# Kernel optimization log

Hardware: AMD Instinct MI355X
Metric: run time of the kernel (lower is better)

Reference implementation:

```python
import jax, jax.numpy as jnp
import numpy as np

N_NODES = 100_000
N_EDGES = 1_600_000
NEG_SLOPE = 0.2

# layer configs: (in_channels, heads, out_channels, has_proj)
LAYERS = [(193, 8, 16, True), (128, 8, 16, False), (128, 8, 16, False), (128, 8, 8, True)]


def _gat_params(key, fin, H, C):
    ks = jax.random.split(key, 6)
    s = 1.0 / np.sqrt(fin)
    Wl = jax.random.normal(ks[0], (fin, H * C), dtype=jnp.float32) * s
    bl = jax.random.normal(ks[1], (H * C,), dtype=jnp.float32) * 0.01
    Wr = jax.random.normal(ks[2], (fin, H * C), dtype=jnp.float32) * s
    br = jax.random.normal(ks[3], (H * C,), dtype=jnp.float32) * 0.01
    att = jax.random.normal(ks[4], (H, C), dtype=jnp.float32) * (1.0 / np.sqrt(C))
    bias = jax.random.normal(ks[5], (H * C,), dtype=jnp.float32) * 0.01
    return Wl, bl, Wr, br, att, bias


def setup_inputs() -> dict:
    key = jax.random.key(0)
    ks = jax.random.split(key, 16)
    inp = {}
    inp['x'] = jax.random.normal(ks[0], (N_NODES, 193), dtype=jnp.float32)
    inp['edge_index'] = jax.random.randint(ks[1], (2, N_EDGES), 0, N_NODES, dtype=jnp.int64)
    for li, (fin, H, C, _) in enumerate(LAYERS, start=1):
        Wl, bl, Wr, br, att, bias = _gat_params(ks[1 + li], fin, H, C)
        inp[f'Wl{li}'] = Wl; inp[f'bl{li}'] = bl
        inp[f'Wr{li}'] = Wr; inp[f'br{li}'] = br
        inp[f'att{li}'] = att; inp[f'bias{li}'] = bias
    # residual projections where in_channels != heads*out_channels
    inp['proj1_W'] = jax.random.normal(ks[8], (193, 128), dtype=jnp.float32) * (1.0 / np.sqrt(193))
    inp['proj1_b'] = jax.random.normal(ks[9], (128,), dtype=jnp.float32) * 0.01
    inp['proj4_W'] = jax.random.normal(ks[10], (128, 64), dtype=jnp.float32) * (1.0 / np.sqrt(128))
    inp['proj4_b'] = jax.random.normal(ks[11], (64,), dtype=jnp.float32) * 0.01
    inp['lin1_W'] = jax.random.normal(ks[12], (64, 32), dtype=jnp.float32) * (1.0 / np.sqrt(64))
    inp['lin1_b'] = jax.random.normal(ks[13], (32,), dtype=jnp.float32) * 0.01
    return inp


def _gatv2(x, src, dst, Wl, bl, Wr, br, att, bias):
    # x: [N, Fin]; att: [H, C]
    N = x.shape[0]
    H, C = att.shape
    xl = (x @ Wl + bl).reshape(N, H, C)  # source transform
    xr = (x @ Wr + br).reshape(N, H, C)  # destination transform
    m = xl[src] + xr[dst]                # [E, H, C] edge gather
    e = jnp.einsum('ehc,hc->eh', jax.nn.leaky_relu(m, NEG_SLOPE), att)  # [E, H]
    emax = jax.ops.segment_max(e, dst, num_segments=N)  # per-dst softmax max
    p = jnp.exp(e - emax[dst])
    denom = jax.ops.segment_sum(p, dst, num_segments=N)
    alpha = p / (denom[dst] + 1e-16)     # [E, H]
    out = jax.ops.segment_sum(alpha[:, :, None] * xl[src], dst, num_segments=N)  # [N, H, C]
    return out.reshape(N, H * C) + bias


def _forward(x, edge_index, params):
    src, dst = edge_index[0], edge_index[1]
    h = x
    for li in range(4):
        Wl, bl, Wr, br, att, bias, projW, projb = params[li]
        g = _gatv2(h, src, dst, Wl, bl, Wr, br, att, bias)
        res = h @ projW + projb if projW is not None else h
        h = jax.nn.gelu(g + res, approximate=False)
    Wf, bf = params[4]
    return h @ Wf + bf


def reference(x, edge_index,
              Wl1, bl1, Wr1, br1, att1, bias1,
              Wl2, bl2, Wr2, br2, att2, bias2,
              Wl3, bl3, Wr3, br3, att3, bias3,
              Wl4, bl4, Wr4, br4, att4, bias4,
              proj1_W, proj1_b, proj4_W, proj4_b, lin1_W, lin1_b):
    params = [
        (Wl1, bl1, Wr1, br1, att1, bias1, proj1_W, proj1_b),
        (Wl2, bl2, Wr2, br2, att2, bias2, None, None),
        (Wl3, bl3, Wr3, br3, att3, bias3, None, None),
        (Wl4, bl4, Wr4, br4, att4, bias4, proj4_W, proj4_b),
        (lin1_W, lin1_b),
    ]
    return _forward(x, edge_index, params)
```

## Files before the change

kernel.cpp:

```cpp
#include <hip/hip_runtime.h>
#include <hip/hip_bf16.h>

#define NNODES 100000

typedef short s16x8 __attribute__((ext_vector_type(8)));
typedef float f32x4 __attribute__((ext_vector_type(4)));

__device__ inline ushort f2bf(float f) {
    uint u = __float_as_uint(f);
    uint r = u + 0x7fffu + ((u >> 16) & 1u);
    return (ushort)(r >> 16);
}
__device__ inline float bf2f(ushort u) { return __uint_as_float(((uint)u) << 16); }
__device__ inline float bflo(uint u) { return __uint_as_float(u << 16); }
__device__ inline float bfhi(uint u) { return __uint_as_float(u & 0xffff0000u); }

__global__ void hist_kernel(const int* __restrict__ dst, int E, int* __restrict__ deg) {
    int e = blockIdx.x * blockDim.x + threadIdx.x;
    if (e < E) atomicAdd(&deg[dst[e]], 1);
}

__global__ __launch_bounds__(256) void scan_part(const int* __restrict__ deg,
                                                 int* __restrict__ bsum, int n) {
    int t = threadIdx.x;
    int base = blockIdx.x * 1024 + t * 4;
    int4 v = make_int4(0, 0, 0, 0);
    if (base + 3 < n) v = *(const int4*)(deg + base);
    else {
        if (base + 0 < n) v.x = deg[base + 0];
        if (base + 1 < n) v.y = deg[base + 1];
        if (base + 2 < n) v.z = deg[base + 2];
    }
    int s = v.x + v.y + v.z + v.w;
#pragma unroll
    for (int o = 1; o < 64; o <<= 1) s += __shfl_xor(s, o);
    __shared__ int ws[4];
    if ((t & 63) == 0) ws[t >> 6] = s;
    __syncthreads();
    if (t == 0) bsum[blockIdx.x] = ws[0] + ws[1] + ws[2] + ws[3];
}

__global__ __launch_bounds__(128) void scan_bsum(int* __restrict__ bsum, int nb,
                                                 int* __restrict__ rowptr, int n) {
    __shared__ int s[128];
    int t = threadIdx.x;
    int v = (t < nb) ? bsum[t] : 0;
    s[t] = v;
    __syncthreads();
#pragma unroll
    for (int o = 1; o < 128; o <<= 1) {
        int u = (t >= o) ? s[t - o] : 0;
        __syncthreads();
        s[t] += u;
        __syncthreads();
    }
    if (t < nb) bsum[t] = s[t] - v;
    if (t == 127) rowptr[n] = s[127];
}

__global__ __launch_bounds__(256) void scan_apply(const int* __restrict__ deg,
                                                  const int* __restrict__ bsum,
                                                  int* __restrict__ rowptr, int n) {
    int t = threadIdx.x;
    int base = blockIdx.x * 1024 + t * 4;
    int4 v = make_int4(0, 0, 0, 0);
    if (base + 3 < n) v = *(const int4*)(deg + base);
    else {
        if (base + 0 < n) v.x = deg[base + 0];
        if (base + 1 < n) v.y = deg[base + 1];
        if (base + 2 < n) v.z = deg[base + 2];
    }
    int s = v.x + v.y + v.z + v.w;
    int lane = t & 63, w = t >> 6;
    int incl = s;
#pragma unroll
    for (int o = 1; o < 64; o <<= 1) {
        int u = __shfl_up(incl, o);
        if (lane >= o) incl += u;
    }
    __shared__ int wsum[4];
    if (lane == 63) wsum[w] = incl;
    __syncthreads();
    int woff = 0;
    if (w > 0) woff += wsum[0];
    if (w > 1) woff += wsum[1];
    if (w > 2) woff += wsum[2];
    int off = bsum[blockIdx.x] + woff + (incl - s);
    int4 r;
    r.x = off;
    r.y = off + v.x;
    r.z = r.y + v.y;
    r.w = r.z + v.z;
    if (base + 3 < n) *(int4*)(rowptr + base) = r;
    else {
        if (base + 0 < n) rowptr[base + 0] = r.x;
        if (base + 1 < n) rowptr[base + 1] = r.y;
        if (base + 2 < n) rowptr[base + 2] = r.z;
    }
}

__global__ void scatter_kernel(const int* __restrict__ src, const int* __restrict__ dst, int E,
                               const int* __restrict__ rowptr, int* __restrict__ cursor,
                               int* __restrict__ csr) {
    int e = blockIdx.x * blockDim.x + threadIdx.x;
    if (e < E) {
        int d = dst[e];
        int pos = rowptr[d] + atomicAdd(&cursor[d], 1);
        csr[pos] = src[e];
    }
}

struct WConvDesc { const float* W; ushort* Wt; int K, N, Kp; };
struct WConvArgs { WConvDesc d[10]; };

__global__ void convert_weights(WConvArgs args) {
    WConvDesc dd = args.d[blockIdx.y];
    int total = dd.N * dd.Kp;
    for (int i = blockIdx.x * 256 + threadIdx.x; i < total; i += gridDim.x * 256) {
        int n = i / dd.Kp, k = i - n * dd.Kp;
        float v = (k < dd.K) ? dd.W[(size_t)k * dd.N + n] : 0.f;
        dd.Wt[i] = f2bf(v);
    }
}

__global__ void convert_x(const float* __restrict__ x, ushort* __restrict__ xb, int M) {
    int total = M * 56;
    for (int i = blockIdx.x * 256 + threadIdx.x; i < total; i += gridDim.x * 256) {
        int n = i / 56;
        int k4 = (i - n * 56) * 4;
        ushort o[4];
#pragma unroll
        for (int j = 0; j < 4; ++j) {
            int k = k4 + j;
            o[j] = (k < 193) ? f2bf(x[(size_t)n * 193 + k]) : (ushort)0;
        }
        *(uint2*)(xb + (size_t)n * 224 + k4) = *(const uint2*)o;
    }
}

#define LP 40
template <int BN>
__global__ __launch_bounds__(256) void gemm_mfma(const ushort* __restrict__ A,
                                                 const ushort* __restrict__ Bt,
                                                 const float* __restrict__ bias,
                                                 ushort* __restrict__ C,
                                                 int M, int Kp, int Cstride, int col0) {
    __shared__ ushort As[128 * LP];
    __shared__ ushort Bs[BN * LP];
    const int t = threadIdx.x;
    const int r0 = blockIdx.x * 128;
    const int lane = t & 63;
    const int w = t >> 6;
    const int la = lane & 15;
    const int lk = (lane >> 4) * 8;

    constexpr int MR = (BN == 128) ? 4 : 2;
    const int m0 = (BN == 128) ? (w >> 1) * 64 : w * 32;
    const int n0 = (BN == 128) ? (w & 1) * 64 : 0;

    f32x4 acc[MR][4];
#pragma unroll
    for (int i = 0; i < MR; ++i)
#pragma unroll
        for (int j = 0; j < 4; ++j) acc[i][j] = (f32x4)0.f;

    const int sr = t >> 1;
    const int skh = (t & 1) * 16;
    const ushort* Ap = A + (size_t)(r0 + sr) * Kp;
    const bool rowok = (r0 + sr) < M;

    for (int k0 = 0; k0 < Kp; k0 += 32) {
        uint4 a0 = make_uint4(0u, 0u, 0u, 0u), a1 = a0;
        if (rowok) {
            const ushort* p = Ap + k0 + skh;
            a0 = ((const uint4*)p)[0];
            a1 = ((const uint4*)p)[1];
        }
        *(uint4*)&As[sr * LP + skh] = a0;
        *(uint4*)&As[sr * LP + skh + 8] = a1;
        if (BN == 128) {
            const ushort* Bp = Bt + (size_t)sr * Kp + k0 + skh;
            *(uint4*)&Bs[sr * LP + skh] = ((const uint4*)Bp)[0];
            *(uint4*)&Bs[sr * LP + skh + 8] = ((const uint4*)Bp)[1];
        } else {
            int nr = t >> 2, kq = (t & 3) * 8;
            const ushort* Bp = Bt + (size_t)nr * Kp + k0 + kq;
            *(uint4*)&Bs[nr * LP + kq] = *(const uint4*)Bp;
        }
        __syncthreads();
        s16x8 av[MR], bv[4];
#pragma unroll
        for (int i = 0; i < MR; ++i)
            av[i] = *(const s16x8*)&As[(m0 + i * 16 + la) * LP + lk];
#pragma unroll
        for (int j = 0; j < 4; ++j)
            bv[j] = *(const s16x8*)&Bs[(n0 + j * 16 + la) * LP + lk];
#pragma unroll
        for (int i = 0; i < MR; ++i)
#pragma unroll
            for (int j = 0; j < 4; ++j)
                acc[i][j] = __builtin_amdgcn_mfma_f32_16x16x32_bf16(av[i], bv[j], acc[i][j], 0, 0, 0);
        __syncthreads();
    }
    const int lrow = (lane >> 4) * 4;
#pragma unroll
    for (int i = 0; i < MR; ++i) {
#pragma unroll
        for (int j = 0; j < 4; ++j) {
            int col = n0 + j * 16 + la;
            float bval = bias[col];
#pragma unroll
            for (int r = 0; r < 4; ++r) {
                int row = r0 + m0 + i * 16 + lrow + r;
                if (row < M) C[(size_t)row * Cstride + col0 + col] = f2bf(acc[i][j][r] + bval);
            }
        }
    }
}

template <int CPL, bool RBF16>
__global__ __launch_bounds__(256) void gat_agg(const ushort* __restrict__ xcat, int xstride,
                                               int xr_off,
                                               const void* __restrict__ resv, int rstride, int roff,
                                               const float* __restrict__ att,
                                               const float* __restrict__ bias,
                                               const int* __restrict__ rowptr,
                                               const int* __restrict__ csr,
                                               float* __restrict__ hout, int hstride,
                                               ushort* __restrict__ houtb, int M) {
    int n = blockIdx.x * 4 + (threadIdx.x >> 6);
    if (n >= M) return;
    const int lane = threadIdx.x & 63;
    const int half = lane >> 5;
    const int c = lane & 31;

    float xr[CPL], at[CPL];
    if (CPL == 4) {
        uint2 u = *(const uint2*)(xcat + (size_t)n * xstride + xr_off + 4 * c);
        xr[0] = bflo(u.x); xr[1] = bfhi(u.x); xr[2] = bflo(u.y); xr[3] = bfhi(u.y);
        float4 a = *(const float4*)(att + 4 * c);
        at[0] = a.x; at[1] = a.y; at[2] = a.z; at[3] = a.w;
    } else {
        uint u = *(const uint*)(xcat + (size_t)n * xstride + xr_off + 2 * c);
        xr[0] = bflo(u); xr[1] = bfhi(u);
        float2 a = *(const float2*)(att + 2 * c);
        at[0] = a.x; at[1] = a.y;
    }

    const int s0 = rowptr[n], s1 = rowptr[n + 1];
    float ssum = 0.f;
    float acc[CPL];
#pragma unroll
    for (int j = 0; j < CPL; ++j) acc[j] = 0.f;

    for (int cs = s0; cs < s1; cs += 64) {
        const int cnt = min(64, s1 - cs);
        const int pairs = (cnt + 1) >> 1;
        const int ci = csr[min(cs + lane, s1 - 1)];

        auto ISSUE = [&](uint2& buf, bool& v, int p) {
            if (p >= pairs) { v = false; buf.x = 0u; buf.y = 0u; return; }
            int idx = 2 * p + half;
            v = idx < cnt;
            int src = __shfl(ci, min(idx, cnt - 1));
            const ushort* rp = xcat + (size_t)src * xstride + ((CPL == 4) ? 4 * c : 2 * c);
            if (CPL == 4) buf = *(const uint2*)rp;
            else          buf.x = *(const uint*)rp;
        };
        auto COMPUTE = [&](const uint2& buf, bool v) {
            float x[CPL];
            x[0] = bflo(buf.x); x[1] = bfhi(buf.x);
            if (CPL == 4) { x[2] = bflo(buf.y); x[3] = bfhi(buf.y); }
            float prod;
            {
                float l[CPL];
#pragma unroll
                for (int j = 0; j < CPL; ++j) {
                    float vv = x[j] + xr[j];
                    l[j] = fmaxf(vv, 0.2f * vv);
                }
                prod = l[0] * at[0];
#pragma unroll
                for (int j = 1; j < CPL; ++j) prod = fmaf(l[j], at[j], prod);
            }
            prod += __shfl_xor(prod, 1);
            prod += __shfl_xor(prod, 2);
            float pe = v ? __expf(prod) : 0.f;
            ssum += pe;
#pragma unroll
            for (int j = 0; j < CPL; ++j) acc[j] = fmaf(pe, x[j], acc[j]);
        };

        uint2 b0, b1, b2, b3, b4, b5, b6, b7;
        bool v0, v1, v2, v3, v4, v5, v6, v7;
        ISSUE(b0, v0, 0); ISSUE(b1, v1, 1); ISSUE(b2, v2, 2); ISSUE(b3, v3, 3);
        ISSUE(b4, v4, 4); ISSUE(b5, v5, 5); ISSUE(b6, v6, 6); ISSUE(b7, v7, 7);
        for (int p = 0; p < pairs; p += 8) {
            COMPUTE(b0, v0); ISSUE(b0, v0, p + 8);
            if (p + 1 < pairs) { COMPUTE(b1, v1); ISSUE(b1, v1, p + 9); }
            if (p + 2 < pairs) { COMPUTE(b2, v2); ISSUE(b2, v2, p + 10); }
            if (p + 3 < pairs) { COMPUTE(b3, v3); ISSUE(b3, v3, p + 11); }
            if (p + 4 < pairs) { COMPUTE(b4, v4); ISSUE(b4, v4, p + 12); }
            if (p + 5 < pairs) { COMPUTE(b5, v5); ISSUE(b5, v5, p + 13); }
            if (p + 6 < pairs) { COMPUTE(b6, v6); ISSUE(b6, v6, p + 14); }
            if (p + 7 < pairs) { COMPUTE(b7, v7); ISSUE(b7, v7, p + 15); }
        }
    }

    ssum += __shfl_xor(ssum, 32);
#pragma unroll
    for (int j = 0; j < CPL; ++j) acc[j] += __shfl_xor(acc[j], 32);

    if (half == 0) {
        float inv = 1.f / (ssum + 1e-16f);
        float r[CPL], bb[CPL], o[CPL];
        if (CPL == 4) {
            if (RBF16) {
                uint2 u = *(const uint2*)((const ushort*)resv + (size_t)n * rstride + roff + 4 * c);
                r[0] = bflo(u.x); r[1] = bfhi(u.x); r[2] = bflo(u.y); r[3] = bfhi(u.y);
            } else {
                float4 rr = *(const float4*)((const float*)resv + (size_t)n * rstride + roff + 4 * c);
                r[0] = rr.x; r[1] = rr.y; r[2] = rr.z; r[3] = rr.w;
            }
            float4 b4v = *(const float4*)(bias + 4 * c);
            bb[0] = b4v.x; bb[1] = b4v.y; bb[2] = b4v.z; bb[3] = b4v.w;
        } else {
            if (RBF16) {
                uint u = *(const uint*)((const ushort*)resv + (size_t)n * rstride + roff + 2 * c);
                r[0] = bflo(u); r[1] = bfhi(u);
            } else {
                float2 rr = *(const float2*)((const float*)resv + (size_t)n * rstride + roff + 2 * c);
                r[0] = rr.x; r[1] = rr.y;
            }
            float2 b2v = *(const float2*)(bias + 2 * c);
            bb[0] = b2v.x; bb[1] = b2v.y;
        }
#pragma unroll
        for (int j = 0; j < CPL; ++j) {
            float y = fmaf(acc[j], inv, bb[j] + r[j]);
            o[j] = 0.5f * y * (1.f + erff(y * 0.70710678118654752f));
        }
        if (CPL == 4) {
            if (hout)
                *(float4*)(hout + (size_t)n * hstride + 4 * c) = make_float4(o[0], o[1], o[2], o[3]);
            if (houtb) {
                uint2 pk;
                pk.x = (uint)f2bf(o[0]) | ((uint)f2bf(o[1]) << 16);
                pk.y = (uint)f2bf(o[2]) | ((uint)f2bf(o[3]) << 16);
                *(uint2*)(houtb + (size_t)n * 128 + 4 * c) = pk;
            }
        } else {
            if (hout)
                *(float2*)(hout + (size_t)n * hstride + 2 * c) = make_float2(o[0], o[1]);
            if (houtb) {
                uint pk = (uint)f2bf(o[0]) | ((uint)f2bf(o[1]) << 16);
                *(uint*)(houtb + (size_t)n * 64 + 2 * c) = pk;
            }
        }
    }
}

__global__ __launch_bounds__(256) void final_linear(const float* __restrict__ h,
                                                    const float* __restrict__ W,
                                                    const float* __restrict__ b,
                                                    float* __restrict__ out, int M) {
    __shared__ float Ws[64 * 32];
    __shared__ float bs[32];
    __shared__ float hs[8][64];
    int t = threadIdx.x;
    for (int i = t; i < 64 * 32; i += 256) Ws[i] = W[i];
    if (t < 32) bs[t] = b[t];
    int r0 = blockIdx.x * 8;
    for (int i = t; i < 8 * 64; i += 256) {
        int r = i >> 6, c = i & 63;
        hs[r][c] = (r0 + r < M) ? h[(size_t)(r0 + r) * 64 + c] : 0.f;
    }
    __syncthreads();
    int lr = t >> 5;
    int col = t & 31;
    int row = r0 + lr;
    if (row >= M) return;
    float acc = bs[col];
#pragma unroll 8
    for (int k = 0; k < 64; ++k) acc += hs[lr][k] * Ws[k * 32 + col];
    out[(size_t)row * 32 + col] = acc;
}

extern "C" void kernel_launch(void* const* d_in, const int* in_sizes, int n_in,
                              void* d_out, int out_size, void* d_ws, size_t ws_size,
                              hipStream_t stream) {
    const float* x = (const float*)d_in[0];
    const int* ei = (const int*)d_in[1];
    const int E = in_sizes[1] / 2;
    const int* srcp = ei;
    const int* dstp = ei + E;

    const float* Wl[4]  = {(const float*)d_in[2],  (const float*)d_in[8],  (const float*)d_in[14], (const float*)d_in[20]};
    const float* bl[4]  = {(const float*)d_in[3],  (const float*)d_in[9],  (const float*)d_in[15], (const float*)d_in[21]};
    const float* Wr[4]  = {(const float*)d_in[4],  (const float*)d_in[10], (const float*)d_in[16], (const float*)d_in[22]};
    const float* br[4]  = {(const float*)d_in[5],  (const float*)d_in[11], (const float*)d_in[17], (const float*)d_in[23]};
    const float* att[4] = {(const float*)d_in[6],  (const float*)d_in[12], (const float*)d_in[18], (const float*)d_in[24]};
    const float* bia[4] = {(const float*)d_in[7],  (const float*)d_in[13], (const float*)d_in[19], (const float*)d_in[25]};
    const float* proj1W = (const float*)d_in[26];
    const float* proj1b = (const float*)d_in[27];
    const float* proj4W = (const float*)d_in[28];
    const float* proj4b = (const float*)d_in[29];
    const float* linW   = (const float*)d_in[30];
    const float* linb   = (const float*)d_in[31];

    const int M = NNODES;
    ushort* xcat = (ushort*)d_ws;
    ushort* xb   = xcat + (size_t)M * 384;
    ushort* hb   = xb;
    float* h  = (float*)(xb + (size_t)M * 224);
    float* h4 = h + (size_t)M * 128;
    ushort* wb = (ushort*)(h4 + (size_t)M * 64);
    ushort* WtL1 = wb; wb += 128 * 224;
    ushort* WtR1 = wb; wb += 128 * 224;
    ushort* WtP1 = wb; wb += 128 * 224;
    ushort* WtL2 = wb; wb += 128 * 128;
    ushort* WtR2 = wb; wb += 128 * 128;
    ushort* WtL3 = wb; wb += 128 * 128;
    ushort* WtR3 = wb; wb += 128 * 128;
    ushort* WtL4 = wb; wb += 64 * 128;
    ushort* WtR4 = wb; wb += 64 * 128;
    ushort* WtP4 = wb; wb += 64 * 128;
    int* deg    = (int*)wb;
    int* cursor = deg + M;
    int* rowptr = cursor + M;
    int* csr    = rowptr + (M + 1);
    int* bsum   = csr + E;

    const int NB = (M + 1023) / 1024;

    hipMemsetAsync(deg, 0, 2 * (size_t)M * sizeof(int), stream);
    hist_kernel<<<(E + 255) / 256, 256, 0, stream>>>(dstp, E, deg);
    scan_part<<<NB, 256, 0, stream>>>(deg, bsum, M);
    scan_bsum<<<1, 128, 0, stream>>>(bsum, NB, rowptr, M);
    scan_apply<<<NB, 256, 0, stream>>>(deg, bsum, rowptr, M);
    scatter_kernel<<<(E + 255) / 256, 256, 0, stream>>>(srcp, dstp, E, rowptr, cursor, csr);

    WConvArgs wa;
    wa.d[0] = {Wl[0],  WtL1, 193, 128, 224};
    wa.d[1] = {Wr[0],  WtR1, 193, 128, 224};
    wa.d[2] = {proj1W, WtP1, 193, 128, 224};
    wa.d[3] = {Wl[1],  WtL2, 128, 128, 128};
    wa.d[4] = {Wr[1],  WtR2, 128, 128, 128};
    wa.d[5] = {Wl[2],  WtL3, 128, 128, 128};
    wa.d[6] = {Wr[2],  WtR3, 128, 128, 128};
    wa.d[7] = {Wl[3],  WtL4, 128, 64, 128};
    wa.d[8] = {Wr[3],  WtR4, 128, 64, 128};
    wa.d[9] = {proj4W, WtP4, 128, 64, 128};
    convert_weights<<<dim3(112, 10), 256, 0, stream>>>(wa);
    convert_x<<<2048, 256, 0, stream>>>(x, xb, M);

    dim3 gg((M + 127) / 128, 1);
    dim3 ag((M + 3) / 4, 1);

    gemm_mfma<128><<<gg, 256, 0, stream>>>(xb, WtL1, bl[0], xcat, M, 224, 384, 0);
    gemm_mfma<128><<<gg, 256, 0, stream>>>(xb, WtR1, br[0], xcat, M, 224, 384, 128);
    gemm_mfma<128><<<gg, 256, 0, stream>>>(xb, WtP1, proj1b, xcat, M, 224, 384, 256);
    gat_agg<4, true><<<ag, 256, 0, stream>>>(xcat, 384, 128, xcat, 384, 256, att[0], bia[0],
                                             rowptr, csr, h, 128, hb, M);
    gemm_mfma<128><<<gg, 256, 0, stream>>>(hb, WtL2, bl[1], xcat, M, 128, 256, 0);
    gemm_mfma<128><<<gg, 256, 0, stream>>>(hb, WtR2, br[1], xcat, M, 128, 256, 128);
    gat_agg<4, false><<<ag, 256, 0, stream>>>(xcat, 256, 128, h, 128, 0, att[1], bia[1],
                                              rowptr, csr, h, 128, hb, M);
    gemm_mfma<128><<<gg, 256, 0, stream>>>(hb, WtL3, bl[2], xcat, M, 128, 256, 0);
    gemm_mfma<128><<<gg, 256, 0, stream>>>(hb, WtR3, br[2], xcat, M, 128, 256, 128);
    gat_agg<4, false><<<ag, 256, 0, stream>>>(xcat, 256, 128, h, 128, 0, att[2], bia[2],
                                              rowptr, csr, nullptr, 128, hb, M);
    gemm_mfma<64><<<gg, 256, 0, stream>>>(hb, WtL4, bl[3], xcat, M, 128, 192, 0);
    gemm_mfma<64><<<gg, 256, 0, stream>>>(hb, WtR4, br[3], xcat, M, 128, 192, 64);
    gemm_mfma<64><<<gg, 256, 0, stream>>>(hb, WtP4, proj4b, xcat, M, 128, 192, 128);
    gat_agg<2, true><<<ag, 256, 0, stream>>>(xcat, 192, 64, xcat, 192, 128, att[3], bia[3],
                                             rowptr, csr, h4, 64, nullptr, M);
    final_linear<<<(M + 7) / 8, 256, 0, stream>>>(h4, linW, linb, (float*)d_out, M);
}
```

Measured before the change: 748.6 us.

## Widen GAT aggregation gathers to 16-byte loads and merge per-layer GEMMs

The aggregation kernel now has each lane load 8 bf16 channels (uint4) per neighbor instead of 2-4, so one wavefront processes 4 or 8 edges at a time. Each lane reads its CSR index directly instead of broadcasting through shuffles, and partial sums are combined with a butterfly reduction at the end. Separately, the Wl/Wr/proj GEMMs of each layer are merged into one launch by concatenating the transposed weights and biases and using blockIdx.y to pick the column block. This aims for fewer, wider gather transactions and fewer kernel launches, at the cost of more cross-lane shuffle reductions and a somewhat more register-heavy per-lane epilogue.

```diff
diff --git a/kernel.cpp b/kernel.cpp
--- a/kernel.cpp
+++ b/kernel.cpp
@@ -123,6 +123,13 @@
     }
 }
 
+struct BCat { const float* src; float* dst; int len; };
+struct BCatArgs { BCat d[10]; };
+__global__ void concat_bias(BCatArgs a) {
+    BCat dd = a.d[blockIdx.x];
+    for (int i = threadIdx.x; i < dd.len; i += 256) dd.dst[i] = dd.src[i];
+}
+
 __global__ void convert_x(const float* __restrict__ x, ushort* __restrict__ xb, int M) {
     int total = M * 56;
     for (int i = blockIdx.x * 256 + threadIdx.x; i < total; i += gridDim.x * 256) {
@@ -141,10 +148,14 @@
 #define LP 40
 template <int BN>
 __global__ __launch_bounds__(256) void gemm_mfma(const ushort* __restrict__ A,
-                                                 const ushort* __restrict__ Bt,
-                                                 const float* __restrict__ bias,
+                                                 const ushort* __restrict__ BtAll,
+                                                 const float* __restrict__ biasAll,
                                                  ushort* __restrict__ C,
-                                                 int M, int Kp, int Cstride, int col0) {
+                                                 int M, int Kp, int Cstride) {
+    const int col0 = blockIdx.y * BN;
+    const ushort* Bt = BtAll + (size_t)col0 * Kp;
+    const float* bias = biasAll + col0;
+
     __shared__ ushort As[128 * LP];
     __shared__ ushort Bs[BN * LP];
     const int t = threadIdx.x;
@@ -218,7 +229,7 @@
     }
 }
 
-template <int CPL, bool RBF16>
+template <int HC, bool RBF16>
 __global__ __launch_bounds__(256) void gat_agg(const ushort* __restrict__ xcat, int xstride,
                                                int xr_off,
                                                const void* __restrict__ resv, int rstride, int roff,
@@ -228,135 +239,109 @@
                                                const int* __restrict__ csr,
                                                float* __restrict__ hout, int hstride,
                                                ushort* __restrict__ houtb, int M) {
-    int n = blockIdx.x * 4 + (threadIdx.x >> 6);
+    constexpr int LPE = HC / 8;
+    constexpr int EPI = 64 / LPE;
+    constexpr int QSH = (HC == 128) ? 4 : 3;
+    const int n = blockIdx.x * 4 + (threadIdx.x >> 6);
     if (n >= M) return;
     const int lane = threadIdx.x & 63;
-    const int half = lane >> 5;
-    const int c = lane & 31;
-
-    float xr[CPL], at[CPL];
-    if (CPL == 4) {
-        uint2 u = *(const uint2*)(xcat + (size_t)n * xstride + xr_off + 4 * c);
+    const int clane = lane & (LPE - 1);
+    const int q = lane >> QSH;
+
+    const char* xb = (const char*)xcat;
+    const uint xrowB = (uint)xstride * 2u;
+    const uint chB = (uint)clane * 16u;
+
+    float xr[8], at[8];
+    {
+        uint4 u = *(const uint4*)(xb + (uint)n * xrowB + (uint)xr_off * 2u + chB);
         xr[0] = bflo(u.x); xr[1] = bfhi(u.x); xr[2] = bflo(u.y); xr[3] = bfhi(u.y);
-        float4 a = *(const float4*)(att + 4 * c);
-        at[0] = a.x; at[1] = a.y; at[2] = a.z; at[3] = a.w;
-    } else {
-        uint u = *(const uint*)(xcat + (size_t)n * xstride + xr_off + 2 * c);
-        xr[0] = bflo(u); xr[1] = bfhi(u);
-        float2 a = *(const float2*)(att + 2 * c);
-        at[0] = a.x; at[1] = a.y;
+        xr[4] = bflo(u.z); xr[5] = bfhi(u.z); xr[6] = bflo(u.w); xr[7] = bfhi(u.w);
+        float4 a0 = *(const float4*)(att + 8 * clane);
+        float4 a1 = *(const float4*)(att + 8 * clane + 4);
+        at[0] = a0.x; at[1] = a0.y; at[2] = a0.z; at[3] = a0.w;
+        at[4] = a1.x; at[5] = a1.y; at[6] = a1.z; at[7] = a1.w;
     }
 
     const int s0 = rowptr[n], s1 = rowptr[n + 1];
     float ssum = 0.f;
-    float acc[CPL];
-#pragma unroll
-    for (int j = 0; j < CPL; ++j) acc[j] = 0.f;
-
-    for (int cs = s0; cs < s1; cs += 64) {
-        const int cnt = min(64, s1 - cs);
-        const int pairs = (cnt + 1) >> 1;
-        const int ci = csr[min(cs + lane, s1 - 1)];
-
-        auto ISSUE = [&](uint2& buf, bool& v, int p) {
-            if (p >= pairs) { v = false; buf.x = 0u; buf.y = 0u; return; }
-            int idx = 2 * p + half;
-            v = idx < cnt;
-            int src = __shfl(ci, min(idx, cnt - 1));
-            const ushort* rp = xcat + (size_t)src * xstride + ((CPL == 4) ? 4 * c : 2 * c);
-            if (CPL == 4) buf = *(const uint2*)rp;
-            else          buf.x = *(const uint*)rp;
+    float acc[8] = {0.f, 0.f, 0.f, 0.f, 0.f, 0.f, 0.f, 0.f};
+
+    if (s1 > s0) {
+        const int nq = (s1 - s0 + EPI - 1) >> (6 - QSH);
+        auto ISSUE = [&](uint4& buf, bool& val, int p) {
+            if (p >= nq) { val = false; buf = make_uint4(0u, 0u, 0u, 0u); return; }
+            int g = s0 + p * EPI + q;
+            val = g < s1;
+            int src = csr[min(g, s1 - 1)];
+            buf = *(const uint4*)(xb + (uint)src * xrowB + chB);
         };
-        auto COMPUTE = [&](const uint2& buf, bool v) {
-            float x[CPL];
-            x[0] = bflo(buf.x); x[1] = bfhi(buf.x);
-            if (CPL == 4) { x[2] = bflo(buf.y); x[3] = bfhi(buf.y); }
-            float prod;
-            {
-                float l[CPL];
-#pragma unroll
-                for (int j = 0; j < CPL; ++j) {
-                    float vv = x[j] + xr[j];
-                    l[j] = fmaxf(vv, 0.2f * vv);
-                }
-                prod = l[0] * at[0];
-#pragma unroll
-                for (int j = 1; j < CPL; ++j) prod = fmaf(l[j], at[j], prod);
+        auto COMPUTE = [&](const uint4& buf, bool val) {
+            float x[8];
+            x[0] = bflo(buf.x); x[1] = bfhi(buf.x); x[2] = bflo(buf.y); x[3] = bfhi(buf.y);
+            x[4] = bflo(buf.z); x[5] = bfhi(buf.z); x[6] = bflo(buf.w); x[7] = bfhi(buf.w);
+            float prod = 0.f;
+#pragma unroll
+            for (int j = 0; j < 8; ++j) {
+                float v = x[j] + xr[j];
+                float l = fmaxf(v, 0.2f * v);
+                prod = fmaf(l, at[j], prod);
             }
-            prod += __shfl_xor(prod, 1);
-            prod += __shfl_xor(prod, 2);
-            float pe = v ? __expf(prod) : 0.f;
+            if constexpr (HC == 128) prod += __shfl_xor(prod, 1);
+            float pe = val ? __expf(prod) : 0.f;
             ssum += pe;
 #pragma unroll
-            for (int j = 0; j < CPL; ++j) acc[j] = fmaf(pe, x[j], acc[j]);
+            for (int j = 0; j < 8; ++j) acc[j] = fmaf(pe, x[j], acc[j]);
         };
-
-        uint2 b0, b1, b2, b3, b4, b5, b6, b7;
-        bool v0, v1, v2, v3, v4, v5, v6, v7;
+        uint4 b0, b1, b2, b3;
+        bool v0, v1, v2, v3;
         ISSUE(b0, v0, 0); ISSUE(b1, v1, 1); ISSUE(b2, v2, 2); ISSUE(b3, v3, 3);
-        ISSUE(b4, v4, 4); ISSUE(b5, v5, 5); ISSUE(b6, v6, 6); ISSUE(b7, v7, 7);
-        for (int p = 0; p < pairs; p += 8) {
-            COMPUTE(b0, v0); ISSUE(b0, v0, p + 8);
-            if (p + 1 < pairs) { COMPUTE(b1, v1); ISSUE(b1, v1, p + 9); }
-            if (p + 2 < pairs) { COMPUTE(b2, v2); ISSUE(b2, v2, p + 10); }
-            if (p + 3 < pairs) { COMPUTE(b3, v3); ISSUE(b3, v3, p + 11); }
-            if (p + 4 < pairs) { COMPUTE(b4, v4); ISSUE(b4, v4, p + 12); }
-            if (p + 5 < pairs) { COMPUTE(b5, v5); ISSUE(b5, v5, p + 13); }
-            if (p + 6 < pairs) { COMPUTE(b6, v6); ISSUE(b6, v6, p + 14); }
-            if (p + 7 < pairs) { COMPUTE(b7, v7); ISSUE(b7, v7, p + 15); }
-        }
-    }
-
-    ssum += __shfl_xor(ssum, 32);
-#pragma unroll
-    for (int j = 0; j < CPL; ++j) acc[j] += __shfl_xor(acc[j], 32);
-
-    if (half == 0) {
-        float inv = 1.f / (ssum + 1e-16f);
-        float r[CPL], bb[CPL], o[CPL];
-        if (CPL == 4) {
-            if (RBF16) {
-                uint2 u = *(const uint2*)((const ushort*)resv + (size_t)n * rstride + roff + 4 * c);
-                r[0] = bflo(u.x); r[1] = bfhi(u.x); r[2] = bflo(u.y); r[3] = bfhi(u.y);
-            } else {
-                float4 rr = *(const float4*)((const float*)resv + (size_t)n * rstride + roff + 4 * c);
-                r[0] = rr.x; r[1] = rr.y; r[2] = rr.z; r[3] = rr.w;
-            }
-            float4 b4v = *(const float4*)(bias + 4 * c);
-            bb[0] = b4v.x; bb[1] = b4v.y; bb[2] = b4v.z; bb[3] = b4v.w;
+        for (int p = 0; p < nq; p += 4) {
+            COMPUTE(b0, v0); ISSUE(b0, v0, p + 4);
+            if (p + 1 < nq) { COMPUTE(b1, v1); ISSUE(b1, v1, p + 5); }
+            if (p + 2 < nq) { COMPUTE(b2, v2); ISSUE(b2, v2, p + 6); }
+            if (p + 3 < nq) { COMPUTE(b3, v3); ISSUE(b3, v3, p + 7); }
+        }
+    }
+
+#pragma unroll
+    for (int o = LPE; o < 64; o <<= 1) {
+        ssum += __shfl_xor(ssum, o);
+#pragma unroll
+        for (int j = 0; j < 8; ++j) acc[j] += __shfl_xor(acc[j], o);
+    }
+
+    float inv = 1.f / (ssum + 1e-16f);
+    if constexpr (HC == 128) {
+        int ch = 8 * clane + 2 * q;
+        float a0s = (q == 0) ? acc[0] : (q == 1) ? acc[2] : (q == 2) ? acc[4] : acc[6];
+        float a1s = (q == 0) ? acc[1] : (q == 1) ? acc[3] : (q == 2) ? acc[5] : acc[7];
+        float r0v, r1v;
+        if (RBF16) {
+            uint u = *(const uint*)((const ushort*)resv + (size_t)n * rstride + roff + ch);
+            r0v = bflo(u); r1v = bfhi(u);
         } else {
-            if (RBF16) {
-                uint u = *(const uint*)((const ushort*)resv + (size_t)n * rstride + roff + 2 * c);
-                r[0] = bflo(u); r[1] = bfhi(u);
-            } else {
-                float2 rr = *(const float2*)((const float*)resv + (size_t)n * rstride + roff + 2 * c);
-                r[0] = rr.x; r[1] = rr.y;
-            }
-            float2 b2v = *(const float2*)(bias + 2 * c);
-            bb[0] = b2v.x; bb[1] = b2v.y;
-        }
-#pragma unroll
-        for (int j = 0; j < CPL; ++j) {
-            float y = fmaf(acc[j], inv, bb[j] + r[j]);
-            o[j] = 0.5f * y * (1.f + erff(y * 0.70710678118654752f));
-        }
-        if (CPL == 4) {
-            if (hout)
-                *(float4*)(hout + (size_t)n * hstride + 4 * c) = make_float4(o[0], o[1], o[2], o[3]);
-            if (houtb) {
-                uint2 pk;
-                pk.x = (uint)f2bf(o[0]) | ((uint)f2bf(o[1]) << 16);
-                pk.y = (uint)f2bf(o[2]) | ((uint)f2bf(o[3]) << 16);
-                *(uint2*)(houtb + (size_t)n * 128 + 4 * c) = pk;
-            }
-        } else {
-            if (hout)
-                *(float2*)(hout + (size_t)n * hstride + 2 * c) = make_float2(o[0], o[1]);
-            if (houtb) {
-                uint pk = (uint)f2bf(o[0]) | ((uint)f2bf(o[1]) << 16);
-                *(uint*)(houtb + (size_t)n * 64 + 2 * c) = pk;
-            }
-        }
+            float2 rr = *(const float2*)((const float*)resv + (size_t)n * rstride + roff + ch);
+            r0v = rr.x; r1v = rr.y;
+        }
+        float2 b2 = *(const float2*)(bias + ch);
+        float y0 = fmaf(a0s, inv, b2.x + r0v);
+        float y1 = fmaf(a1s, inv, b2.y + r1v);
+        float o0 = 0.5f * y0 * (1.f + erff(y0 * 0.70710678118654752f));
+        float o1 = 0.5f * y1 * (1.f + erff(y1 * 0.70710678118654752f));
+        if (hout) *(float2*)(hout + (size_t)n * hstride + ch) = make_float2(o0, o1);
+        if (houtb) *(uint*)(houtb + (size_t)n * HC + ch) = (uint)f2bf(o0) | ((uint)f2bf(o1) << 16);
+    } else {
+        int ch = 8 * clane + q;
+        float a0s = (q == 0) ? acc[0] : (q == 1) ? acc[1] : (q == 2) ? acc[2] : (q == 3) ? acc[3]
+                  : (q == 4) ? acc[4] : (q == 5) ? acc[5] : (q == 6) ? acc[6] : acc[7];
+        float r0v;
+        if (RBF16) r0v = bf2f(((const ushort*)resv)[(size_t)n * rstride + roff + ch]);
+        else       r0v = ((const float*)resv)[(size_t)n * rstride + roff + ch];
+        float y0 = fmaf(a0s, inv, bias[ch] + r0v);
+        float o0 = 0.5f * y0 * (1.f + erff(y0 * 0.70710678118654752f));
+        if (hout) hout[(size_t)n * hstride + ch] = o0;
+        if (houtb) houtb[(size_t)n * HC + ch] = f2bf(o0);
     }
 }
 
@@ -415,17 +400,15 @@
     float* h  = (float*)(xb + (size_t)M * 224);
     float* h4 = h + (size_t)M * 128;
     ushort* wb = (ushort*)(h4 + (size_t)M * 64);
-    ushort* WtL1 = wb; wb += 128 * 224;
-    ushort* WtR1 = wb; wb += 128 * 224;
-    ushort* WtP1 = wb; wb += 128 * 224;
-    ushort* WtL2 = wb; wb += 128 * 128;
-    ushort* WtR2 = wb; wb += 128 * 128;
-    ushort* WtL3 = wb; wb += 128 * 128;
-    ushort* WtR3 = wb; wb += 128 * 128;
-    ushort* WtL4 = wb; wb += 64 * 128;
-    ushort* WtR4 = wb; wb += 64 * 128;
-    ushort* WtP4 = wb; wb += 64 * 128;
-    int* deg    = (int*)wb;
+    ushort* WtC1 = wb; wb += 384 * 224;
+    ushort* WtC2 = wb; wb += 256 * 128;
+    ushort* WtC3 = wb; wb += 256 * 128;
+    ushort* WtC4 = wb; wb += 192 * 128;
+    float* bc1 = (float*)wb;
+    float* bc2 = bc1 + 384;
+    float* bc3 = bc2 + 256;
+    float* bc4 = bc3 + 256;
+    int* deg    = (int*)(bc4 + 192);
     int* cursor = deg + M;
     int* rowptr = cursor + M;
     int* csr    = rowptr + (M + 1);
@@ -441,39 +424,45 @@
     scatter_kernel<<<(E + 255) / 256, 256, 0, stream>>>(srcp, dstp, E, rowptr, cursor, csr);
 
     WConvArgs wa;
-    wa.d[0] = {Wl[0],  WtL1, 193, 128, 224};
-    wa.d[1] = {Wr[0],  WtR1, 193, 128, 224};
-    wa.d[2] = {proj1W, WtP1, 193, 128, 224};
-    wa.d[3] = {Wl[1],  WtL2, 128, 128, 128};
-    wa.d[4] = {Wr[1],  WtR2, 128, 128, 128};
-    wa.d[5] = {Wl[2],  WtL3, 128, 128, 128};
-    wa.d[6] = {Wr[2],  WtR3, 128, 128, 128};
-    wa.d[7] = {Wl[3],  WtL4, 128, 64, 128};
-    wa.d[8] = {Wr[3],  WtR4, 128, 64, 128};
-    wa.d[9] = {proj4W, WtP4, 128, 64, 128};
+    wa.d[0] = {Wl[0],  WtC1,             193, 128, 224};
+    wa.d[1] = {Wr[0],  WtC1 + 128 * 224, 193, 128, 224};
+    wa.d[2] = {proj1W, WtC1 + 256 * 224, 193, 128, 224};
+    wa.d[3] = {Wl[1],  WtC2,             128, 128, 128};
+    wa.d[4] = {Wr[1],  WtC2 + 128 * 128, 128, 128, 128};
+    wa.d[5] = {Wl[2],  WtC3,             128, 128, 128};
+    wa.d[6] = {Wr[2],  WtC3 + 128 * 128, 128, 128, 128};
+    wa.d[7] = {Wl[3],  WtC4,             128, 64, 128};
+    wa.d[8] = {Wr[3],  WtC4 + 64 * 128,  128, 64, 128};
+    wa.d[9] = {proj4W, WtC4 + 128 * 128, 128, 64, 128};
     convert_weights<<<dim3(112, 10), 256, 0, stream>>>(wa);
+    BCatArgs ba;
+    ba.d[0] = {bl[0],  bc1,       128};
+    ba.d[1] = {br[0],  bc1 + 128, 128};
+    ba.d[2] = {proj1b, bc1 + 256, 128};
+    ba.d[3] = {bl[1],  bc2,       128};
+    ba.d[4] = {br[1],  bc2 + 128, 128};
+    ba.d[5] = {bl[2],  bc3,       128};
+    ba.d[6] = {br[2],  bc3 + 128, 128};
+    ba.d[7] = {bl[3],  bc4,       64};
+    ba.d[8] = {br[3],  bc4 + 64,  64};
+    ba.d[9] = {proj4b, bc4 + 128, 64};
+    concat_bias<<<10, 256, 0, stream>>>(ba);
     convert_x<<<2048, 256, 0, stream>>>(x, xb, M);
 
-    dim3 gg((M + 127) / 128, 1);
+    const int GX = (M + 127) / 128;
     dim3 ag((M + 3) / 4, 1);
 
-    gemm_mfma<128><<<gg, 256, 0, stream>>>(xb, WtL1, bl[0], xcat, M, 224, 384, 0);
-    gemm_mfma<128><<<gg, 256, 0, stream>>>(xb, WtR1, br[0], xcat, M, 224, 384, 128);
-    gemm_mfma<128><<<gg, 256, 0, stream>>>(xb, WtP1, proj1b, xcat, M, 224, 384, 256);
-    gat_agg<4, true><<<ag, 256, 0, stream>>>(xcat, 384, 128, xcat, 384, 256, att[0], bia[0],
-                                             rowptr, csr, h, 128, hb, M);
-    gemm_mfma<128><<<gg, 256, 0, stream>>>(hb, WtL2, bl[1], xcat, M, 128, 256, 0);
-    gemm_mfma<128><<<gg, 256, 0, stream>>>(hb, WtR2, br[1], xcat, M, 128, 256, 128);
-    gat_agg<4, false><<<ag, 256, 0, stream>>>(xcat, 256, 128, h, 128, 0, att[1], bia[1],
-                                              rowptr, csr, h, 128, hb, M);
-    gemm_mfma<128><<<gg, 256, 0, stream>>>(hb, WtL3, bl[2], xcat, M, 128, 256, 0);
-    gemm_mfma<128><<<gg, 256, 0, stream>>>(hb, WtR3, br[2], xcat, M, 128, 256, 128);
-    gat_agg<4, false><<<ag, 256, 0, stream>>>(xcat, 256, 128, h, 128, 0, att[2], bia[2],
-                                              rowptr, csr, nullptr, 128, hb, M);
-    gemm_mfma<64><<<gg, 256, 0, stream>>>(hb, WtL4, bl[3], xcat, M, 128, 192, 0);
-    gemm_mfma<64><<<gg, 256, 0, stream>>>(hb, WtR4, br[3], xcat, M, 128, 192, 64);
-    gemm_mfma<64><<<gg, 256, 0, stream>>>(hb, WtP4, proj4b, xcat, M, 128, 192, 128);
-    gat_agg<2, true><<<ag, 256, 0, stream>>>(xcat, 192, 64, xcat, 192, 128, att[3], bia[3],
-                                             rowptr, csr, h4, 64, nullptr, M);
+    gemm_mfma<128><<<dim3(GX, 3), 256, 0, stream>>>(xb, WtC1, bc1, xcat, M, 224, 384);
+    gat_agg<128, true><<<ag, 256, 0, stream>>>(xcat, 384, 128, xcat, 384, 256, att[0], bia[0],
+                                               rowptr, csr, h, 128, hb, M);
+    gemm_mfma<128><<<dim3(GX, 2), 256, 0, stream>>>(hb, WtC2, bc2, xcat, M, 128, 256);
+    gat_agg<128, false><<<ag, 256, 0, stream>>>(xcat, 256, 128, h, 128, 0, att[1], bia[1],
+                                                rowptr, csr, h, 128, hb, M);
+    gemm_mfma<128><<<dim3(GX, 2), 256, 0, stream>>>(hb, WtC3, bc3, xcat, M, 128, 256);
+    gat_agg<128, false><<<ag, 256, 0, stream>>>(xcat, 256, 128, h, 128, 0, att[2], bia[2],
+                                                rowptr, csr, nullptr, 128, hb, M);
+    gemm_mfma<64><<<dim3(GX, 3), 256, 0, stream>>>(hb, WtC4, bc4, xcat, M, 128, 192);
+    gat_agg<64, true><<<ag, 256, 0, stream>>>(xcat, 192, 64, xcat, 192, 128, att[3], bia[3],
+                                              rowptr, csr, h4, 64, nullptr, M);
     final_linear<<<(M + 7) / 8, 256, 0, stream>>>(h4, linW, linb, (float*)d_out, M);
 }
```

New measurement: 681.7 us. 1.1x faster.
